# Performance work log

Measured on AMD Instinct MI355X. Metric: run time of the kernel, lower is better.

Reference implementation:

```python
import jax, jax.numpy as jnp
import numpy as np

N_NODES = 20000
N_EDGES = 1280000
IN_CH = 256
HID_CH = 256


def setup_inputs() -> dict:
    key = jax.random.key(0)
    ks = jax.random.split(key, 8)
    s = 1.0 / np.sqrt(IN_CH)
    sh = 1.0 / np.sqrt(HID_CH)
    return {
        "x": jax.random.normal(ks[0], (N_NODES, IN_CH), dtype=jnp.float32),
        "edge_index": jax.random.randint(ks[1], (2, N_EDGES), 0, N_NODES, dtype=jnp.int64),
        "W1_l": jax.random.normal(ks[2], (HID_CH, IN_CH), dtype=jnp.float32) * s,
        "b1": jnp.zeros((HID_CH,), dtype=jnp.float32),
        "W1_r": jax.random.normal(ks[3], (HID_CH, IN_CH), dtype=jnp.float32) * s,
        "W2_l": jax.random.normal(ks[4], (1, HID_CH), dtype=jnp.float32) * sh,
        "b2": jnp.zeros((1,), dtype=jnp.float32),
        "W2_r": jax.random.normal(ks[5], (1, HID_CH), dtype=jnp.float32) * sh,
        "fc_w": jax.random.normal(ks[6], (1, N_NODES), dtype=jnp.float32) * (1.0 / np.sqrt(N_NODES)),
        "fc_b": jnp.zeros((1,), dtype=jnp.float32),
    }


def _sage(x, src, dst, inv_deg, W_l, b, W_r):
    # mean-aggregate source features at destination nodes, then two linears
    agg = jax.ops.segment_sum(x[src], dst, num_segments=N_NODES)  # [N, C]
    mean = agg * inv_deg[:, None]
    return mean @ W_l.T + b + x @ W_r.T


def reference(x, edge_index, W1_l, b1, W1_r, W2_l, b2, W2_r, fc_w, fc_b):
    src, dst = edge_index[0], edge_index[1]
    deg = jax.ops.segment_sum(jnp.ones((dst.shape[0],), dtype=x.dtype), dst,
                              num_segments=N_NODES)
    inv_deg = 1.0 / jnp.maximum(deg, 1.0)  # isolated nodes -> 0 aggregate
    h = jax.nn.relu(_sage(x, src, dst, inv_deg, W1_l, b1, W1_r))   # [N, H]
    h = jax.nn.relu(_sage(h, src, dst, inv_deg, W2_l, b2, W2_r))   # [N, 1]
    h = h[:, 0]                                                     # squeeze dim 1
    return h @ fc_w[0] + fc_b                                       # [1]
```

## Files before the change

### kernel.cpp

```cpp
#include <hip/hip_runtime.h>

#define N_NODESC 20000
#define N_EDGESC 1280000
#define NB 256
#define EPB 5000

typedef short bf16x8 __attribute__((ext_vector_type(8)));
typedef float f32x4 __attribute__((ext_vector_type(4)));

constexpr size_t OFF_DEG      = 0;
constexpr size_t OFF_ROWSTART = 81920;
constexpr size_t OFF_INVDEG   = 163840;
constexpr size_t OFF_BSUM     = 245760;
constexpr size_t OFF_BOFF     = 246272;
constexpr size_t OFF_S1       = 246784;
constexpr size_t OFF_T1       = 326784;
constexpr size_t OFF_PART     = 406784;
constexpr size_t OFF_HIST     = 427264;
constexpr size_t OFF_CSR      = 10667264;
constexpr size_t OFF_XB       = 13227392;
constexpr size_t OFF_MEANB    = 23467392;
constexpr size_t OFF_W1LB     = 33707392;
constexpr size_t OFF_W1RB     = 33838464;

static __device__ __forceinline__ unsigned f2bf(float f) {
    unsigned u = __float_as_uint(f);
    return ((u + 0x7fffu + ((u >> 16) & 1u)) >> 16) & 0xffffu;
}
static __device__ __forceinline__ float bflo(unsigned w) {
    return __uint_as_float(w << 16);
}
static __device__ __forceinline__ float bfhi(unsigned w) {
    return __uint_as_float(w & 0xffff0000u);
}

__global__ void __launch_bounds__(256) k_cast(
        const float4* __restrict__ x, const float4* __restrict__ w1l,
        const float4* __restrict__ w1r, uint4* __restrict__ xb,
        uint4* __restrict__ w1lb, uint4* __restrict__ w1rb,
        float* __restrict__ s1, float* __restrict__ t1,
        int* __restrict__ bsum) {
    int g = blockIdx.x * 256 + threadIdx.x;
    if (g < N_NODESC) { s1[g] = 0.0f; t1[g] = 0.0f; }
    if (g < 128) bsum[g] = 0;
    const float4* src; uint4* dst; int off;
    if (g < 640000)      { src = x;   dst = xb;   off = g; }
    else if (g < 648192) { src = w1l; dst = w1lb; off = g - 640000; }
    else                 { src = w1r; dst = w1rb; off = g - 648192; }
    float4 a = src[off * 2], b = src[off * 2 + 1];
    uint4 o;
    o.x = f2bf(a.x) | (f2bf(a.y) << 16);
    o.y = f2bf(a.z) | (f2bf(a.w) << 16);
    o.z = f2bf(b.x) | (f2bf(b.y) << 16);
    o.w = f2bf(b.z) | (f2bf(b.w) << 16);
    dst[off] = o;
}

__global__ void __launch_bounds__(256) k_hist(const int* __restrict__ ei,
                                              unsigned short* __restrict__ hist) {
    __shared__ unsigned int lh[10000];
    int b = blockIdx.x, t = threadIdx.x;
    for (int w = t; w < 10000; w += 256) lh[w] = 0;
    __syncthreads();
    int base = b * EPB;
    for (int i = t; i < EPB; i += 256) {
        int d = ei[N_EDGESC + base + i];
        atomicAdd(&lh[d >> 1], (d & 1) ? 0x10000u : 1u);
    }
    __syncthreads();
    unsigned int* gh = (unsigned int*)(hist + (size_t)b * N_NODESC);
    for (int w = t; w < 10000; w += 256) gh[w] = lh[w];
}

__global__ void __launch_bounds__(256) k_prefix(unsigned short* __restrict__ hist,
                                                int* __restrict__ deg,
                                                int* __restrict__ bsum) {
    __shared__ int wtot[4][64];
    int t = threadIdx.x;
    int lb = t & 63, sub = t >> 6;
    int bin = blockIdx.x * 64 + lb;
    bool ok = bin < N_NODESC;
    int vals[64];
    int run = 0;
    if (ok) {
        #pragma unroll
        for (int i = 0; i < 64; i++) {
            vals[i] = hist[(size_t)(sub * 64 + i) * N_NODESC + bin];
            run += vals[i];
        }
    }
    wtot[sub][lb] = run;
    __syncthreads();
    int off = 0, total = 0;
    for (int w = 0; w < 4; w++) {
        int v = wtot[w][lb];
        if (w < sub) off += v;
        total += v;
    }
    if (sub == 0) {
        int tv = ok ? total : 0;
        if (ok) deg[bin] = total;
        #pragma unroll
        for (int o2 = 32; o2 > 0; o2 >>= 1) tv += __shfl_down(tv, o2);
        if (lb == 0) atomicAdd(&bsum[(blockIdx.x * 64) >> 8], tv);
    }
    if (ok) {
        int run2 = off;
        #pragma unroll
        for (int i = 0; i < 64; i++) {
            hist[(size_t)(sub * 64 + i) * N_NODESC + bin] = (unsigned short)run2;
            run2 += vals[i];
        }
    }
}

__global__ void k_scan2(const int* __restrict__ bsum, int* __restrict__ boff,
                        int* __restrict__ row_start) {
    __shared__ int sm[128];
    int t = threadIdx.x;
    int v = (t < 79) ? bsum[t] : 0;
    sm[t] = v;
    __syncthreads();
    for (int off = 1; off < 128; off <<= 1) {
        int add = (t >= off) ? sm[t - off] : 0;
        __syncthreads();
        sm[t] += add;
        __syncthreads();
    }
    if (t < 79) boff[t] = sm[t] - v;
    if (t == 0) row_start[N_NODESC] = sm[127];
}

__global__ void __launch_bounds__(256) k_scan3(
        const int* __restrict__ deg, const int* __restrict__ boff,
        int* __restrict__ row_start, float* __restrict__ inv_deg) {
    __shared__ int wsum[4];
    int i = blockIdx.x * 256 + threadIdx.x;
    int lane = threadIdx.x & 63, wid = threadIdx.x >> 6;
    int v = (i < N_NODESC) ? deg[i] : 0;
    int incl = v;
    #pragma unroll
    for (int off = 1; off < 64; off <<= 1) {
        int n = __shfl_up(incl, off);
        if (lane >= off) incl += n;
    }
    if (lane == 63) wsum[wid] = incl;
    __syncthreads();
    int wpre = 0;
    #pragma unroll
    for (int w = 0; w < 4; w++) wpre += (w < wid) ? wsum[w] : 0;
    if (i < N_NODESC) {
        row_start[i] = boff[blockIdx.x] + wpre + incl - v;
        inv_deg[i]   = 1.0f / (float)max(v, 1);
    }
}

__global__ void __launch_bounds__(256) k_fill2(const int* __restrict__ ei,
        const int* __restrict__ row_start, const unsigned short* __restrict__ hist,
        unsigned short* __restrict__ csr) {
    __shared__ unsigned int lh[10000];
    int b = blockIdx.x, t = threadIdx.x;
    for (int w = t; w < 10000; w += 256) lh[w] = 0;
    __syncthreads();
    int base = b * EPB;
    const unsigned short* hb = hist + (size_t)b * N_NODESC;
    for (int i = t; i < EPB; i += 256) {
        int e = base + i;
        int d = ei[N_EDGESC + e];
        int s = ei[e];
        unsigned int old = atomicAdd(&lh[d >> 1], (d & 1) ? 0x10000u : 1u);
        int rank = (d & 1) ? (int)(old >> 16) : (int)(old & 0xffffu);
        int pos = row_start[d] + (int)hb[d] + rank;
        csr[pos] = (unsigned short)s;
    }
}

__global__ void __launch_bounds__(256) k_agg(const uint2* __restrict__ xb2,
        const int* __restrict__ row_start, const unsigned short* __restrict__ csr,
        const float* __restrict__ inv_deg, uint2* __restrict__ meanb2) {
    int wid = threadIdx.x >> 6, lane = threadIdx.x & 63;
    int node = blockIdx.x * 4 + wid;
    int start = row_start[node], end = row_start[node + 1];
    float a0 = 0.f, a1 = 0.f, a2 = 0.f, a3 = 0.f;
    float c0 = 0.f, c1 = 0.f, c2 = 0.f, c3 = 0.f;
    int idx = (start < end) ? (int)csr[start + lane] : 0;
    for (int j = start; j < end; j += 64) {
        int cnt = min(64, end - j);
        int idxn = (j + 64 < end) ? (int)csr[j + 64 + lane] : 0;
        int k = 0;
        for (; k + 16 <= cnt; k += 16) {
            #pragma unroll
            for (int u = 0; u < 16; u += 2) {
                int s0 = __builtin_amdgcn_readlane(idx, k + u);
                int s1 = __builtin_amdgcn_readlane(idx, k + u + 1);
                uint2 v0 = xb2[(size_t)s0 * 64 + lane];
                uint2 v1 = xb2[(size_t)s1 * 64 + lane];
                a0 += bflo(v0.x); a1 += bfhi(v0.x);
                a2 += bflo(v0.y); a3 += bfhi(v0.y);
                c0 += bflo(v1.x); c1 += bfhi(v1.x);
                c2 += bflo(v1.y); c3 += bfhi(v1.y);
            }
        }
        for (; k < cnt; k++) {
            int s0 = __builtin_amdgcn_readlane(idx, k);
            uint2 v = xb2[(size_t)s0 * 64 + lane];
            a0 += bflo(v.x); a1 += bfhi(v.x);
            a2 += bflo(v.y); a3 += bfhi(v.y);
        }
        idx = idxn;
    }
    float inv = inv_deg[node];
    uint2 o;
    o.x = f2bf((a0 + c0) * inv) | (f2bf((a1 + c1) * inv) << 16);
    o.y = f2bf((a2 + c2) * inv) | (f2bf((a3 + c3) * inv) << 16);
    meanb2[(size_t)node * 64 + lane] = o;
}

__global__ void __launch_bounds__(256) k_gemm(const uint4* __restrict__ meanb4,
        const uint4* __restrict__ xb4, const uint4* __restrict__ w1lb4,
        const uint4* __restrict__ w1rb4, const float* __restrict__ b1,
        const float* __restrict__ w2l, const float* __restrict__ w2r,
        float* __restrict__ s1, float* __restrict__ t1) {
    __shared__ __align__(16) unsigned short As[64][72];
    __shared__ __align__(16) unsigned short Bs[64][72];
    int t = threadIdx.x;
    int m0 = blockIdx.x * 64, n0 = blockIdx.y * 64;
    int wv = t >> 6, l = t & 63, lr = l & 15, quad = l >> 4;
    f32x4 acc[4] = {{0,0,0,0},{0,0,0,0},{0,0,0,0},{0,0,0,0}};
    for (int kt = 0; kt < 8; kt++) {
        const uint4* Asrc = (kt < 4) ? meanb4 : xb4;
        const uint4* Bsrc = (kt < 4) ? w1lb4 : w1rb4;
        int k0q = (kt & 3) * 8;
        #pragma unroll
        for (int p = 0; p < 2; p++) {
            int f = t + p * 256;
            int row = f >> 3, cc = f & 7;
            int m = m0 + row;
            uint4 va = (m < N_NODESC) ? Asrc[(size_t)m * 32 + k0q + cc]
                                      : make_uint4(0, 0, 0, 0);
            uint4 vb = Bsrc[(size_t)(n0 + row) * 32 + k0q + cc];
            *(uint4*)&As[row][cc * 8] = va;
            *(uint4*)&Bs[row][cc * 8] = vb;
        }
        __syncthreads();
        #pragma unroll
        for (int ks = 0; ks < 64; ks += 32) {
            bf16x8 af = *(const bf16x8*)&As[wv * 16 + lr][ks + quad * 8];
            #pragma unroll
            for (int jj = 0; jj < 4; jj++) {
                bf16x8 bf = *(const bf16x8*)&Bs[jj * 16 + lr][ks + quad * 8];
                acc[jj] = __builtin_amdgcn_mfma_f32_16x16x32_bf16(
                              af, bf, acc[jj], 0, 0, 0);
            }
        }
        __syncthreads();
    }
    float ps[4] = {0, 0, 0, 0}, pt[4] = {0, 0, 0, 0};
    #pragma unroll
    for (int jj = 0; jj < 4; jj++) {
        int col = n0 + jj * 16 + lr;
        float bb = b1[col], wl = w2l[col], wr = w2r[col];
        #pragma unroll
        for (int r = 0; r < 4; r++) {
            float h = fmaxf(acc[jj][r] + bb, 0.0f);
            ps[r] += h * wl; pt[r] += h * wr;
        }
    }
    #pragma unroll
    for (int r = 0; r < 4; r++) {
        #pragma unroll
        for (int off = 8; off > 0; off >>= 1) {
            ps[r] += __shfl_down(ps[r], off, 16);
            pt[r] += __shfl_down(pt[r], off, 16);
        }
    }
    if (lr == 0) {
        int mb = m0 + wv * 16 + quad * 4;
        #pragma unroll
        for (int r = 0; r < 4; r++) {
            int m = mb + r;
            if (m < N_NODESC) {
                atomicAdd(&s1[m], ps[r]);
                atomicAdd(&t1[m], pt[r]);
            }
        }
    }
}

__global__ void __launch_bounds__(256) k_layer2(
        const int* __restrict__ row_start, const unsigned short* __restrict__ csr,
        const float* __restrict__ inv_deg, const float* __restrict__ s1,
        const float* __restrict__ t1, const float* __restrict__ b2,
        const float* __restrict__ fc_w, float* __restrict__ part) {
    __shared__ float pw[4];
    int wid = threadIdx.x >> 6, lane = threadIdx.x & 63;
    int node = blockIdx.x * 4 + wid;
    float contrib = 0.0f;
    if (node < N_NODESC) {
        int start = row_start[node], end = row_start[node + 1];
        float s = 0.0f;
        for (int j = start + lane; j < end; j += 64) s += s1[csr[j]];
        #pragma unroll
        for (int off = 32; off > 0; off >>= 1) s += __shfl_down(s, off);
        if (lane == 0) {
            float h2 = fmaxf(s * inv_deg[node] + b2[0] + t1[node], 0.0f);
            contrib = h2 * fc_w[node];
        }
    }
    if (lane == 0) pw[wid] = contrib;
    __syncthreads();
    if (threadIdx.x == 0)
        part[blockIdx.x] = pw[0] + pw[1] + pw[2] + pw[3];
}

__global__ void __launch_bounds__(256) k_final(const float* __restrict__ part,
        const float* __restrict__ fc_b, float* __restrict__ out) {
    __shared__ float sm[4];
    int t = threadIdx.x;
    float s = 0.0f;
    for (int i = t; i < 5000; i += 256) s += part[i];
    #pragma unroll
    for (int off = 32; off > 0; off >>= 1) s += __shfl_down(s, off);
    if ((t & 63) == 0) sm[t >> 6] = s;
    __syncthreads();
    if (t == 0) out[0] = sm[0] + sm[1] + sm[2] + sm[3] + fc_b[0];
}

extern "C" void kernel_launch(void* const* d_in, const int* in_sizes, int n_in,
                              void* d_out, int out_size, void* d_ws, size_t ws_size,
                              hipStream_t stream) {
    const float* x    = (const float*)d_in[0];
    const int*   ei   = (const int*)d_in[1];
    const float* w1l  = (const float*)d_in[2];
    const float* b1   = (const float*)d_in[3];
    const float* w1r  = (const float*)d_in[4];
    const float* w2l  = (const float*)d_in[5];
    const float* b2   = (const float*)d_in[6];
    const float* w2r  = (const float*)d_in[7];
    const float* fcw  = (const float*)d_in[8];
    const float* fcb  = (const float*)d_in[9];
    float* out = (float*)d_out;

    char* ws = (char*)d_ws;
    int*    deg       = (int*)(ws + OFF_DEG);
    int*    row_start = (int*)(ws + OFF_ROWSTART);
    float*  inv_deg   = (float*)(ws + OFF_INVDEG);
    int*    bsum      = (int*)(ws + OFF_BSUM);
    int*    boff      = (int*)(ws + OFF_BOFF);
    float*  s1        = (float*)(ws + OFF_S1);
    float*  t1        = (float*)(ws + OFF_T1);
    float*  part      = (float*)(ws + OFF_PART);
    unsigned short* hist = (unsigned short*)(ws + OFF_HIST);
    unsigned short* csr  = (unsigned short*)(ws + OFF_CSR);
    uint2*  xb2       = (uint2*)(ws + OFF_XB);
    uint2*  meanb2    = (uint2*)(ws + OFF_MEANB);
    uint4*  w1lb4     = (uint4*)(ws + OFF_W1LB);
    uint4*  w1rb4     = (uint4*)(ws + OFF_W1RB);

    k_cast<<<2564, 256, 0, stream>>>((const float4*)x, (const float4*)w1l,
                                     (const float4*)w1r, (uint4*)xb2,
                                     w1lb4, w1rb4, s1, t1, bsum);
    k_hist<<<NB, 256, 0, stream>>>(ei, hist);
    k_prefix<<<313, 256, 0, stream>>>(hist, deg, bsum);
    k_scan2<<<1, 128, 0, stream>>>(bsum, boff, row_start);
    k_scan3<<<79, 256, 0, stream>>>(deg, boff, row_start, inv_deg);
    k_fill2<<<NB, 256, 0, stream>>>(ei, row_start, hist, csr);
    k_agg<<<5000, 256, 0, stream>>>((const uint2*)xb2, row_start, csr, inv_deg,
                                    meanb2);
    dim3 ggrid(313, 4);
    k_gemm<<<ggrid, 256, 0, stream>>>((const uint4*)meanb2, (const uint4*)xb2,
                                      (const uint4*)w1lb4, (const uint4*)w1rb4,
                                      b1, w2l, w2r, s1, t1);
    k_layer2<<<5000, 256, 0, stream>>>(row_start, csr, inv_deg, s1, t1, b2,
                                       fcw, part);
    k_final<<<1, 256, 0, stream>>>(part, fcb, out);
}
```

Measured before the change: 233.0 us.

## Split aggregation into four column passes with quad-parallel edge gathering

The mean-aggregation kernel now runs four grid passes, each covering a 128-byte column slice of the bf16 features. Each wavefront splits into four 16-lane quads that gather different neighbours at once, then combines the quads with cross-lane shuffles before writing. Each pass's feature working set is a quarter of the full rows, which is meant to improve L2 hit rate on random neighbour gathers. In exchange, the CSR indices are read four times, there are more blocks, and each row gather is 128-byte rather than 512-byte, which could hurt memory efficiency.

New measurement: 224.0 us. 1.04x faster.

```diff
diff --git a/kernel.cpp b/kernel.cpp
--- a/kernel.cpp
+++ b/kernel.cpp
@@ -180,40 +180,59 @@
         const float* __restrict__ inv_deg, uint2* __restrict__ meanb2) {
     int wid = threadIdx.x >> 6, lane = threadIdx.x & 63;
     int node = blockIdx.x * 4 + wid;
+    int pass = blockIdx.y;
+    int cl = lane & 15, quad = lane >> 4;
     int start = row_start[node], end = row_start[node + 1];
+    const uint2* xq = xb2 + (pass << 4) + cl;
     float a0 = 0.f, a1 = 0.f, a2 = 0.f, a3 = 0.f;
     float c0 = 0.f, c1 = 0.f, c2 = 0.f, c3 = 0.f;
     int idx = (start < end) ? (int)csr[start + lane] : 0;
     for (int j = start; j < end; j += 64) {
         int cnt = min(64, end - j);
         int idxn = (j + 64 < end) ? (int)csr[j + 64 + lane] : 0;
+        int fs = cnt >> 2;
         int k = 0;
-        for (; k + 16 <= cnt; k += 16) {
-            #pragma unroll
-            for (int u = 0; u < 16; u += 2) {
-                int s0 = __builtin_amdgcn_readlane(idx, k + u);
-                int s1 = __builtin_amdgcn_readlane(idx, k + u + 1);
-                uint2 v0 = xb2[(size_t)s0 * 64 + lane];
-                uint2 v1 = xb2[(size_t)s1 * 64 + lane];
-                a0 += bflo(v0.x); a1 += bfhi(v0.x);
-                a2 += bflo(v0.y); a3 += bfhi(v0.y);
-                c0 += bflo(v1.x); c1 += bfhi(v1.x);
-                c2 += bflo(v1.y); c3 += bfhi(v1.y);
+        for (; k + 4 <= fs; k += 4) {
+            int s0 = __shfl(idx, 4 * k + quad);
+            int s1 = __shfl(idx, 4 * k + 4 + quad);
+            int s2 = __shfl(idx, 4 * k + 8 + quad);
+            int s3 = __shfl(idx, 4 * k + 12 + quad);
+            uint2 v0 = xq[(size_t)s0 << 6];
+            uint2 v1 = xq[(size_t)s1 << 6];
+            uint2 v2 = xq[(size_t)s2 << 6];
+            uint2 v3 = xq[(size_t)s3 << 6];
+            a0 += bflo(v0.x); a1 += bfhi(v0.x); a2 += bflo(v0.y); a3 += bfhi(v0.y);
+            c0 += bflo(v1.x); c1 += bfhi(v1.x); c2 += bflo(v1.y); c3 += bfhi(v1.y);
+            a0 += bflo(v2.x); a1 += bfhi(v2.x); a2 += bflo(v2.y); a3 += bfhi(v2.y);
+            c0 += bflo(v3.x); c1 += bfhi(v3.x); c2 += bflo(v3.y); c3 += bfhi(v3.y);
+        }
+        for (; k < fs; k++) {
+            int s0 = __shfl(idx, 4 * k + quad);
+            uint2 v = xq[(size_t)s0 << 6];
+            a0 += bflo(v.x); a1 += bfhi(v.x); a2 += bflo(v.y); a3 += bfhi(v.y);
+        }
+        int rem = cnt & 3;
+        if (rem) {
+            int s0 = __shfl(idx, 4 * fs + quad);
+            if (quad < rem) {
+                uint2 v = xq[(size_t)s0 << 6];
+                c0 += bflo(v.x); c1 += bfhi(v.x); c2 += bflo(v.y); c3 += bfhi(v.y);
             }
         }
-        for (; k < cnt; k++) {
-            int s0 = __builtin_amdgcn_readlane(idx, k);
-            uint2 v = xb2[(size_t)s0 * 64 + lane];
-            a0 += bflo(v.x); a1 += bfhi(v.x);
-            a2 += bflo(v.y); a3 += bfhi(v.y);
-        }
         idx = idxn;
     }
-    float inv = inv_deg[node];
-    uint2 o;
-    o.x = f2bf((a0 + c0) * inv) | (f2bf((a1 + c1) * inv) << 16);
-    o.y = f2bf((a2 + c2) * inv) | (f2bf((a3 + c3) * inv) << 16);
-    meanb2[(size_t)node * 64 + lane] = o;
+    a0 += c0; a1 += c1; a2 += c2; a3 += c3;
+    a0 += __shfl_down(a0, 32); a1 += __shfl_down(a1, 32);
+    a2 += __shfl_down(a2, 32); a3 += __shfl_down(a3, 32);
+    a0 += __shfl_down(a0, 16); a1 += __shfl_down(a1, 16);
+    a2 += __shfl_down(a2, 16); a3 += __shfl_down(a3, 16);
+    if (quad == 0) {
+        float inv = inv_deg[node];
+        uint2 o;
+        o.x = f2bf(a0 * inv) | (f2bf(a1 * inv) << 16);
+        o.y = f2bf(a2 * inv) | (f2bf(a3 * inv) << 16);
+        meanb2[(size_t)node * 64 + (pass << 4) + cl] = o;
+    }
 }
 
 __global__ void __launch_bounds__(256) k_gemm(const uint4* __restrict__ meanb4,
@@ -365,8 +384,9 @@
     k_scan2<<<1, 128, 0, stream>>>(bsum, boff, row_start);
     k_scan3<<<79, 256, 0, stream>>>(deg, boff, row_start, inv_deg);
     k_fill2<<<NB, 256, 0, stream>>>(ei, row_start, hist, csr);
-    k_agg<<<5000, 256, 0, stream>>>((const uint2*)xb2, row_start, csr, inv_deg,
-                                    meanb2);
+    dim3 agrid(5000, 4);
+    k_agg<<<agrid, 256, 0, stream>>>((const uint2*)xb2, row_start, csr, inv_deg,
+                                     meanb2);
     dim3 ggrid(313, 4);
     k_gemm<<<ggrid, 256, 0, stream>>>((const uint4*)meanb2, (const uint4*)xb2,
                                       (const uint4*)w1lb4, (const uint4*)w1rb4,
```
